# Kernel optimization log

Hardware: AMD Instinct MI355X
Metric: run time of the kernel (lower is better)

The kernel has to match this reference:

```python
import jax, jax.numpy as jnp
import numpy as np

BATCH = 8192
FEATS = 4096
RATE = 0.1
ANNEAL = 0.5 + 0.1  # self.anneal = 0.5 + anneal


def setup_inputs() -> dict:
    key = jax.random.key(0)
    k1, k2 = jax.random.split(key)
    inputs = jax.random.normal(k1, (BATCH, FEATS), dtype=jnp.float32)
    # standard-normal draws, one per feature (replaces the serial map_fn RNG)
    noise = jax.random.normal(k2, (FEATS,), dtype=jnp.float32)
    return {"inputs": inputs, "noise": noise}


def reference(inputs, noise):
    # SegDropout (training path), agg_method='mean', noise_type='gaussian'
    F = inputs.shape[-1]
    x_agg = jnp.mean(inputs, axis=0)                      # [F] batch-wise aggregate
    x_min = jnp.min(x_agg)
    x_max = jnp.max(x_agg)
    # quantize each feature's aggregate into one of F+1 integer bins
    bins = (F * (x_agg - x_min) / (x_max - x_min)).astype(jnp.int32)  # [F], values in [0, F]
    # unique_with_counts + gather(counts, idx) == histogram lookup per feature
    counts_per_bin = jnp.bincount(bins, length=F + 1)      # [F+1]
    counts = counts_per_bin[bins].astype(inputs.dtype)     # [F] count of each feature's bin
    dr = RATE ** (1.0 / (ANNEAL * counts))                 # annealed per-bin dropout rate
    dr = jnp.where(counts == 1.0, jnp.asarray(RATE, inputs.dtype), dr)
    sigma = jnp.sqrt(dr / (1.0 - dr))                      # [F]
    # multiplicative Gaussian noise ~ N(1, sigma) per feature
    return inputs * (1.0 + sigma * noise)
```

## Files before the change

### kernel.cpp

```cpp
#include <hip/hip_runtime.h>

#define BATCH 8192
#define FEATS 4096
#define CHUNKS 128
#define ROWS_PER_CHUNK (BATCH / CHUNKS)
#define SROWS 16
#define RBLK 64
#define KSLICES 4
#define KPER (CHUNKS / KSLICES)

typedef float v4f __attribute__((ext_vector_type(4)));


__global__ __launch_bounds__(256) void colsum_part(const float* __restrict__ in,
                                                   double* __restrict__ partials) {
    const int colBase = blockIdx.x * 1024 + threadIdx.x * 4;
    const int row0 = blockIdx.y * ROWS_PER_CHUNK;
    const float4* p = (const float4*)in + (size_t)row0 * (FEATS / 4) + (colBase >> 2);
    double a0 = 0.0, a1 = 0.0, a2 = 0.0, a3 = 0.0;
#pragma unroll 16
    for (int r = 0; r < ROWS_PER_CHUNK; ++r) {
        float4 v = p[(size_t)r * (FEATS / 4)];
        a0 += (double)v.x; a1 += (double)v.y; a2 += (double)v.z; a3 += (double)v.w;
    }
    double* dst = partials + (size_t)blockIdx.y * FEATS + colBase;
    dst[0] = a0; dst[1] = a1; dst[2] = a2; dst[3] = a3;
}

__global__ __launch_bounds__(256) void reduce_mean(const double* __restrict__ partials,
                                                   double* __restrict__ means,
                                                   double* __restrict__ bmin,
                                                   double* __restrict__ bmax) {
    const int t = threadIdx.x;
    const int cLocal = t & 63;
    const int ks = t >> 6;
    const int c = blockIdx.x * 64 + cLocal;

    double s = 0.0;
#pragma unroll 8
    for (int k = 0; k < KPER; ++k)
        s += partials[(size_t)(ks * KPER + k) * FEATS + c];

    __shared__ double sred[KSLICES][64];
    sred[ks][cLocal] = s;
    __syncthreads();

    if (ks == 0) {
        double m = ((sred[0][cLocal] + sred[1][cLocal]) + sred[2][cLocal]) + sred[3][cLocal];
        m *= (1.0 / (double)BATCH);
        means[c] = m;
        double lmin = m, lmax = m;
#pragma unroll
        for (int off = 32; off > 0; off >>= 1) {
            lmin = fmin(lmin, __shfl_down(lmin, off));
            lmax = fmax(lmax, __shfl_down(lmax, off));
        }
        if (cLocal == 0) { bmin[blockIdx.x] = lmin; bmax[blockIdx.x] = lmax; }
    }
}

__global__ __launch_bounds__(1024) void config_kernel(const double* __restrict__ means,
                                                      const double* __restrict__ bmin,
                                                      const double* __restrict__ bmax,
                                                      const float* __restrict__ noise,
                                                      float* __restrict__ scale) {
    __shared__ unsigned s_hist[FEATS + 1];
    __shared__ double s_mm[2];
    const int tid = threadIdx.x;

    if (tid < 64) {
        double a = bmin[tid], b = bmax[tid];
#pragma unroll
        for (int off = 32; off > 0; off >>= 1) {
            a = fmin(a, __shfl_down(a, off));
            b = fmax(b, __shfl_down(b, off));
        }
        if (tid == 0) { s_mm[0] = a; s_mm[1] = b; }
    }
    for (int i = tid; i < FEATS + 1; i += 1024) s_hist[i] = 0;
    __syncthreads();

    const double xmin = s_mm[0];
    const double denom = s_mm[1] - xmin;

    int binr[4];
#pragma unroll
    for (int k = 0; k < 4; ++k) {
        int c = tid + k * 1024;
        double b = ((double)FEATS * (means[c] - xmin)) / denom;
        int bi = (int)b;
        binr[k] = bi;
        atomicAdd(&s_hist[bi], 1u);
    }
    __syncthreads();

    const double K = -2.302585092994045684017991454684364208;
#pragma unroll
    for (int k = 0; k < 4; ++k) {
        int c = tid + k * 1024;
        unsigned cnt = s_hist[binr[k]];
        double dr = (cnt == 1u) ? 0.1 : exp(K / (0.6 * (double)cnt));
        double sg = sqrt(dr / (1.0 - dr));
        scale[c] = (float)(1.0 + sg * (double)noise[c]);
    }
}

__global__ __launch_bounds__(256) void scale_kernel(const float4* __restrict__ in,
                                                    const float4* __restrict__ scale,
                                                    float4* __restrict__ out) {
    const int col = (blockIdx.x & 3) * 256 + threadIdx.x;
    const int row0 = (blockIdx.x >> 2) * SROWS;
    const float4 s = scale[col];
    const float4* pin = in + (size_t)row0 * (FEATS / 4) + col;
    float4* pout = out + (size_t)row0 * (FEATS / 4) + col;
#pragma unroll
    for (int r = 0; r < SROWS; ++r) {
        float4 v = pin[(size_t)r * (FEATS / 4)];
        v.x *= s.x; v.y *= s.y; v.z *= s.z; v.w *= s.w;
        v4f nv = {v.x, v.y, v.z, v.w};
        __builtin_nontemporal_store(nv, (v4f*)&pout[(size_t)r * (FEATS / 4)]);
    }
}

extern "C" void kernel_launch(void* const* d_in, const int* in_sizes, int n_in,
                              void* d_out, int out_size, void* d_ws, size_t ws_size,
                              hipStream_t stream) {
    const float* in = (const float*)d_in[0];
    const float* noise = (const float*)d_in[1];
    float* out = (float*)d_out;
    double* partials = (double*)d_ws;
    double* means = partials + (size_t)CHUNKS * FEATS;
    double* bmin = means + FEATS;
    double* bmax = bmin + RBLK;
    float* scale = (float*)(bmax + RBLK);

    dim3 g1(4, CHUNKS);
    colsum_part<<<g1, 256, 0, stream>>>(in, partials);
    reduce_mean<<<RBLK, 256, 0, stream>>>(partials, means, bmin, bmax);
    config_kernel<<<1, 1024, 0, stream>>>(means, bmin, bmax, noise, scale);
    scale_kernel<<<4 * (BATCH / SROWS), 256, 0, stream>>>(
        (const float4*)in, (const float4*)scale, (float4*)out);
}
```

Measured before the change: 257.5 us.

## Fuse config histogram into scale kernel, recomputing per block

Removes the single-block config kernel and folds min/max, histogram and per-feature scale computation into every block of the scale kernel. Each of the 2048 blocks rereads all 4096 means, builds a 4097-entry shared histogram with atomics, and computes scales for its columns. This drops one launch and the serial single-block stage, but adds a large amount of redundant per-block work and extra shared memory ahead of the streaming loop.

```diff
diff --git a/kernel.cpp b/kernel.cpp
--- a/kernel.cpp
+++ b/kernel.cpp
@@ -28,9 +28,7 @@
 }
 
 __global__ __launch_bounds__(256) void reduce_mean(const double* __restrict__ partials,
-                                                   double* __restrict__ means,
-                                                   double* __restrict__ bmin,
-                                                   double* __restrict__ bmax) {
+                                                   double* __restrict__ means) {
     const int t = threadIdx.x;
     const int cLocal = t & 63;
     const int ks = t >> 6;
@@ -47,72 +45,65 @@
 
     if (ks == 0) {
         double m = ((sred[0][cLocal] + sred[1][cLocal]) + sred[2][cLocal]) + sred[3][cLocal];
-        m *= (1.0 / (double)BATCH);
-        means[c] = m;
-        double lmin = m, lmax = m;
-#pragma unroll
-        for (int off = 32; off > 0; off >>= 1) {
-            lmin = fmin(lmin, __shfl_down(lmin, off));
-            lmax = fmax(lmax, __shfl_down(lmax, off));
-        }
-        if (cLocal == 0) { bmin[blockIdx.x] = lmin; bmax[blockIdx.x] = lmax; }
+        means[c] = m * (1.0 / (double)BATCH);
     }
 }
 
-__global__ __launch_bounds__(1024) void config_kernel(const double* __restrict__ means,
-                                                      const double* __restrict__ bmin,
-                                                      const double* __restrict__ bmax,
-                                                      const float* __restrict__ noise,
-                                                      float* __restrict__ scale) {
+__global__ __launch_bounds__(256) void scale_fused(const float* __restrict__ in,
+                                                   const double* __restrict__ means,
+                                                   const float* __restrict__ noise,
+                                                   float* __restrict__ out) {
     __shared__ unsigned s_hist[FEATS + 1];
-    __shared__ double s_mm[2];
-    const int tid = threadIdx.x;
+    __shared__ double smin[4], smax[4];
+    const int t = threadIdx.x;
 
-    if (tid < 64) {
-        double a = bmin[tid], b = bmax[tid];
+    double lmin = 1e300, lmax = -1e300;
 #pragma unroll
-        for (int off = 32; off > 0; off >>= 1) {
-            a = fmin(a, __shfl_down(a, off));
-            b = fmax(b, __shfl_down(b, off));
-        }
-        if (tid == 0) { s_mm[0] = a; s_mm[1] = b; }
+    for (int k = 0; k < 16; ++k) {
+        double m = means[t + k * 256];
+        lmin = fmin(lmin, m);
+        lmax = fmax(lmax, m);
     }
-    for (int i = tid; i < FEATS + 1; i += 1024) s_hist[i] = 0;
+#pragma unroll
+    for (int off = 32; off > 0; off >>= 1) {
+        lmin = fmin(lmin, __shfl_down(lmin, off));
+        lmax = fmax(lmax, __shfl_down(lmax, off));
+    }
+    if ((t & 63) == 0) { smin[t >> 6] = lmin; smax[t >> 6] = lmax; }
+    for (int i = t; i < FEATS + 1; i += 256) s_hist[i] = 0;
     __syncthreads();
 
-    const double xmin = s_mm[0];
-    const double denom = s_mm[1] - xmin;
+    const double xmin = fmin(fmin(smin[0], smin[1]), fmin(smin[2], smin[3]));
+    const double xmax = fmax(fmax(smax[0], smax[1]), fmax(smax[2], smax[3]));
+    const double denom = xmax - xmin;
 
-    int binr[4];
 #pragma unroll
-    for (int k = 0; k < 4; ++k) {
-        int c = tid + k * 1024;
-        double b = ((double)FEATS * (means[c] - xmin)) / denom;
-        int bi = (int)b;
-        binr[k] = bi;
-        atomicAdd(&s_hist[bi], 1u);
+    for (int k = 0; k < 16; ++k) {
+        double b = ((double)FEATS * (means[t + k * 256] - xmin)) / denom;
+        atomicAdd(&s_hist[(int)b], 1u);
     }
     __syncthreads();
 
+    const int col = (blockIdx.x & 3) * 256 + t;
     const double K = -2.302585092994045684017991454684364208;
+    float4 s;
+    {
+        float sv[4];
 #pragma unroll
-    for (int k = 0; k < 4; ++k) {
-        int c = tid + k * 1024;
-        unsigned cnt = s_hist[binr[k]];
-        double dr = (cnt == 1u) ? 0.1 : exp(K / (0.6 * (double)cnt));
-        double sg = sqrt(dr / (1.0 - dr));
-        scale[c] = (float)(1.0 + sg * (double)noise[c]);
+        for (int j = 0; j < 4; ++j) {
+            const int c = col * 4 + j;
+            double b = ((double)FEATS * (means[c] - xmin)) / denom;
+            unsigned cnt = s_hist[(int)b];
+            double dr = (cnt == 1u) ? 0.1 : exp(K / (0.6 * (double)cnt));
+            double sg = sqrt(dr / (1.0 - dr));
+            sv[j] = (float)(1.0 + sg * (double)noise[c]);
+        }
+        s.x = sv[0]; s.y = sv[1]; s.z = sv[2]; s.w = sv[3];
     }
-}
 
-__global__ __launch_bounds__(256) void scale_kernel(const float4* __restrict__ in,
-                                                    const float4* __restrict__ scale,
-                                                    float4* __restrict__ out) {
-    const int col = (blockIdx.x & 3) * 256 + threadIdx.x;
     const int row0 = (blockIdx.x >> 2) * SROWS;
-    const float4 s = scale[col];
-    const float4* pin = in + (size_t)row0 * (FEATS / 4) + col;
-    float4* pout = out + (size_t)row0 * (FEATS / 4) + col;
+    const float4* pin = (const float4*)in + (size_t)row0 * (FEATS / 4) + col;
+    float4* pout = (float4*)out + (size_t)row0 * (FEATS / 4) + col;
 #pragma unroll
     for (int r = 0; r < SROWS; ++r) {
         float4 v = pin[(size_t)r * (FEATS / 4)];
@@ -130,14 +121,9 @@
     float* out = (float*)d_out;
     double* partials = (double*)d_ws;
     double* means = partials + (size_t)CHUNKS * FEATS;
-    double* bmin = means + FEATS;
-    double* bmax = bmin + RBLK;
-    float* scale = (float*)(bmax + RBLK);
 
     dim3 g1(4, CHUNKS);
     colsum_part<<<g1, 256, 0, stream>>>(in, partials);
-    reduce_mean<<<RBLK, 256, 0, stream>>>(partials, means, bmin, bmax);
-    config_kernel<<<1, 1024, 0, stream>>>(means, bmin, bmax, noise, scale);
-    scale_kernel<<<4 * (BATCH / SROWS), 256, 0, stream>>>(
-        (const float4*)in, (const float4*)scale, (float4*)out);
+    reduce_mean<<<RBLK, 256, 0, stream>>>(partials, means);
+    scale_fused<<<4 * (BATCH / SROWS), 256, 0, stream>>>(in, means, noise, out);
 }
```

After: 257.4 us. Within noise of the previous version (-0.0%).
